# Kernel tuning notes

Hardware: AMD Instinct MI355X
Metric: run time of the kernel (lower is better)

## Reference

```python
import jax, jax.numpy as jnp
import numpy as np

V, E, H, T, B, L = 50000, 512, 1024, 21, 64, 256


def setup_inputs() -> dict:
    key = jax.random.key(0)
    ks = jax.random.split(key, 16)
    s = 0.05
    return {
        "input_ids": jax.random.randint(ks[0], (B, L), 0, V, dtype=jnp.int32),
        "tags": jax.random.randint(ks[1], (B, L), 0, T, dtype=jnp.int32),
        "mask": jnp.ones((B, L), dtype=bool),
        "embed_table": jax.random.normal(ks[2], (V, E), dtype=jnp.float32) * s,
        "W_ih_f": jax.random.normal(ks[3], (4 * H, E), dtype=jnp.float32) * s,
        "W_hh_f": jax.random.normal(ks[4], (4 * H, H), dtype=jnp.float32) * s,
        "b_ih_f": jnp.zeros((4 * H,), jnp.float32),
        "b_hh_f": jnp.zeros((4 * H,), jnp.float32),
        "W_ih_b": jax.random.normal(ks[5], (4 * H, E), dtype=jnp.float32) * s,
        "W_hh_b": jax.random.normal(ks[6], (4 * H, H), dtype=jnp.float32) * s,
        "b_ih_b": jnp.zeros((4 * H,), jnp.float32),
        "b_hh_b": jnp.zeros((4 * H,), jnp.float32),
        "W_out": jax.random.normal(ks[7], (T, 2 * H), dtype=jnp.float32) * s,
        "b_out": jnp.zeros((T,), jnp.float32),
        "start_trans": jax.random.uniform(ks[8], (T,), minval=-0.1, maxval=0.1),
        "end_trans": jax.random.uniform(ks[9], (T,), minval=-0.1, maxval=0.1),
        "transitions": jax.random.uniform(ks[10], (T, T), minval=-0.1, maxval=0.1),
    }


def _lstm_dir(x_proj, W_hh):
    # x_proj: [L, B, 4H] = x @ W_ih.T + b_ih + b_hh. PyTorch gate order i,f,g,o.
    Hh = W_hh.shape[1]
    Bn = x_proj.shape[1]

    def step(carry, xt):
        h, c = carry
        g = xt + h @ W_hh.T
        i, f, gg, o = jnp.split(g, 4, axis=-1)
        c = jax.nn.sigmoid(f) * c + jax.nn.sigmoid(i) * jnp.tanh(gg)
        h = jax.nn.sigmoid(o) * jnp.tanh(c)
        return (h, c), h

    init = (jnp.zeros((Bn, Hh), x_proj.dtype), jnp.zeros((Bn, Hh), x_proj.dtype))
    _, hs = jax.lax.scan(step, init, x_proj)
    return hs  # [L, B, H]


def reference(input_ids, tags, mask, embed_table, W_ih_f, W_hh_f, b_ih_f, b_hh_f,
              W_ih_b, W_hh_b, b_ih_b, b_hh_b, W_out, b_out,
              start_trans, end_trans, transitions):
    # Embedding (padding_idx=0 row is zero in torch)
    emb = embed_table.at[0].set(0.0)[input_ids]          # [B, L, E]
    x = jnp.swapaxes(emb, 0, 1)                          # [L, B, E]

    # BiLSTM: precompute input projections, scan each direction
    hs_f = _lstm_dir(x @ W_ih_f.T + b_ih_f + b_hh_f, W_hh_f)           # [L, B, H]
    hs_b = _lstm_dir(x[::-1] @ W_ih_b.T + b_ih_b + b_hh_b, W_hh_b)[::-1]
    emissions = jnp.concatenate([hs_f, hs_b], axis=-1) @ W_out.T + b_out  # [L, B, T]

    m = jnp.swapaxes(mask, 0, 1).astype(emissions.dtype)  # [L, B]
    tg = jnp.swapaxes(tags, 0, 1)                         # [L, B]

    # CRF numerator: gold path score
    em_t = jnp.take_along_axis(emissions, tg[:, :, None], axis=2)[..., 0]  # [L, B]
    tr_t = transitions[tg[:-1], tg[1:]]                                    # [L-1, B]
    num = start_trans[tg[0]] + em_t[0] + jnp.sum((tr_t + em_t[1:]) * m[1:], axis=0)
    last_idx = jnp.sum(m, axis=0).astype(jnp.int32) - 1                    # [B]
    last_tags = jnp.take_along_axis(tg, last_idx[None, :], axis=0)[0]
    num = num + end_trans[last_tags]

    # CRF partition function: forward algorithm over time
    def step(score, inp):
        em, mm = inp
        nxt = jax.nn.logsumexp(score[:, :, None] + transitions[None] + em[:, None, :], axis=1)
        return jnp.where(mm[:, None] > 0, nxt, score), None

    score0 = start_trans[None, :] + emissions[0]          # [B, T]
    score, _ = jax.lax.scan(step, score0, (emissions[1:], m[1:]))
    logZ = jax.nn.logsumexp(score + end_trans[None, :], axis=1)  # [B]

    # loss = -crf(emissions, tags, mask, reduction='mean')
    return -jnp.mean(num - logZ)
```

## Files before the change

kernel.cpp:

```cpp
#include <hip/hip_runtime.h>
#include <math.h>

#define VV 50000
#define EE 512
#define HH 1024
#define G4 4096
#define NT 21
#define NB 64
#define LL 256
#define KTOT 1536

typedef __attribute__((ext_vector_type(8))) short short8v;
typedef __attribute__((ext_vector_type(4))) float float4v;

__device__ __forceinline__ float sigf(float x){ return 1.f/(1.f+__expf(-x)); }

__device__ __forceinline__ float bf2f(unsigned short u){
  union { unsigned int i; float f; } v; v.i = ((unsigned int)u)<<16; return v.f;
}
__device__ __forceinline__ unsigned short f2bf(float f){
  union { float f; unsigned int u; } v; v.f = f;
  unsigned int u = v.u;
  u += 0x7FFFu + ((u >> 16) & 1u);
  return (unsigned short)(u >> 16);
}


__global__ void k_cast_weights(const float* __restrict__ Wih_f, const float* __restrict__ Whh_f,
                               const float* __restrict__ Wih_b, const float* __restrict__ Whh_b,
                               unsigned short* __restrict__ Wcat)
{
  int idx = blockIdx.x*256 + threadIdx.x;
  if (idx >= 2*4096*192) return;
  int dir = idx / (4096*192);
  int rem = idx - dir*(4096*192);
  int g   = rem / 192;
  int kc  = rem - g*192;
  const float* src;
  if (kc < 64) src = (dir ? Wih_b : Wih_f) + (size_t)g*EE + kc*8;
  else         src = (dir ? Whh_b : Whh_f) + (size_t)g*HH + (kc-64)*8;
  unsigned short tmp[8];
  #pragma unroll
  for (int e=0;e<8;e++) tmp[e] = f2bf(src[e]);
  *(uint4*)(Wcat + (size_t)(dir*G4 + g)*KTOT + kc*8) = *(const uint4*)tmp;
}

__global__ void k_bias(const float* bif, const float* bhf,
                       const float* bib, const float* bhb, float* bsum)
{
  int idx = blockIdx.x*256 + threadIdx.x;
  if (idx >= 2*G4) return;
  int d = idx >> 12, g = idx & (G4-1);
  bsum[idx] = d ? (bib[g]+bhb[g]) : (bif[g]+bhf[g]);
}

__global__ void k_embed(const int* __restrict__ ids, const float* __restrict__ table,
                        unsigned short* __restrict__ x)
{
  int tok = blockIdx.x;
  int t = tok >> 6, b = tok & 63;
  int id = ids[b*LL + t];
  int e0 = threadIdx.x*8;
  unsigned short tmp[8];
  if (id == 0) {
    #pragma unroll
    for (int e=0;e<8;e++) tmp[e] = 0;
  } else {
    const float* row = table + (size_t)id*EE + e0;
    #pragma unroll
    for (int e=0;e<8;e++) tmp[e] = f2bf(row[e]);
  }
  *(uint4*)(x + (size_t)tok*EE + e0) = *(const uint4*)tmp;
}

__global__ void k_zero(unsigned short* hsf0, unsigned short* hsb0, float* cst)
{
  int idx = blockIdx.x*256 + threadIdx.x;
  if (idx < NB*HH) { hsf0[idx] = 0; hsb0[idx] = 0; }
  if (idx < 2*NB*HH) cst[idx] = 0.f;
}

__global__ __launch_bounds__(256) void k_step(
    const unsigned short* __restrict__ Wcat, const float* __restrict__ bsum,
    const unsigned short* __restrict__ x,
    unsigned short* __restrict__ hs_f, unsigned short* __restrict__ hs_b,
    float* __restrict__ cst, int t)
{
  const int dir = blockIdx.x >> 6;
  const int j   = blockIdx.x & 63;
  const int tid = threadIdx.x;
  const int w = tid >> 6, lane = tid & 63;
  const int l15 = lane & 15, lg = lane >> 4;

  const int xtime = dir ? (LL-1 - t) : t;
  unsigned short* hbuf = dir ? hs_b : hs_f;
  const unsigned short* hprev = hbuf + (size_t)t*(NB*HH);
  unsigned short*       hnext = hbuf + (size_t)(t+1)*(NB*HH);
  const unsigned short* xt = x + (size_t)xtime*(NB*EE);

  const int gc0 = w*HH + j*16;
  const short8v* wp = (const short8v*)(Wcat + ((size_t)(dir*G4 + gc0 + l15))*KTOT + lg*8);

  float4v acc[4];
  #pragma unroll
  for (int mt=0;mt<4;mt++)
    #pragma unroll
    for (int i=0;i<4;i++) acc[mt][i] = 0.f;

  #pragma unroll 4
  for (int kt=0; kt<16; kt++) {
    short8v bfrag = wp[kt*4];
    #pragma unroll
    for (int mt=0; mt<4; mt++) {
      short8v afrag = *(const short8v*)(xt + (size_t)(mt*16 + l15)*EE + kt*32 + lg*8);
      acc[mt] = __builtin_amdgcn_mfma_f32_16x16x32_bf16(afrag, bfrag, acc[mt], 0, 0, 0);
    }
  }
  #pragma unroll 4
  for (int kt=0; kt<32; kt++) {
    short8v bfrag = wp[(16+kt)*4];
    #pragma unroll
    for (int mt=0; mt<4; mt++) {
      short8v afrag = *(const short8v*)(hprev + (size_t)(mt*16 + l15)*HH + kt*32 + lg*8);
      acc[mt] = __builtin_amdgcn_mfma_f32_16x16x32_bf16(afrag, bfrag, acc[mt], 0, 0, 0);
    }
  }

  __shared__ float gbuf[4][64][17];
  #pragma unroll
  for (int mt=0;mt<4;mt++)
    #pragma unroll
    for (int i=0;i<4;i++)
      gbuf[w][mt*16 + lg*4 + i][l15] = acc[mt][i];
  __syncthreads();

  const int colbase = j*16;
  #pragma unroll
  for (int k=0;k<4;k++){
    int e  = k*256 + tid;
    int b  = e >> 4, hc = e & 15;
    int col = colbase + hc;
    float gi = gbuf[0][b][hc] + bsum[dir*G4 + col];
    float gf = gbuf[1][b][hc] + bsum[dir*G4 + HH   + col];
    float gg = gbuf[2][b][hc] + bsum[dir*G4 + 2*HH + col];
    float go = gbuf[3][b][hc] + bsum[dir*G4 + 3*HH + col];
    size_t ci = (size_t)dir*(NB*HH) + (size_t)b*HH + col;
    float c0 = cst[ci];
    float cn = sigf(gf)*c0 + sigf(gi)*tanhf(gg);
    float hn = sigf(go)*tanhf(cn);
    cst[ci] = cn;
    hnext[(size_t)b*HH + col] = f2bf(hn);
  }
}

__global__ __launch_bounds__(256) void k_emis(
    const unsigned short* __restrict__ hs_f, const unsigned short* __restrict__ hs_b,
    const float* __restrict__ Wout, const float* __restrict__ bout,
    float* __restrict__ em)
{
  int wid = blockIdx.x*4 + (threadIdx.x >> 6);
  int lane = threadIdx.x & 63;
  int t = wid >> 6, b = wid & 63;

  const unsigned short* hf = hs_f + (size_t)(t+1)*(NB*HH) + (size_t)b*HH + lane*16;
  const unsigned short* hb = hs_b + (size_t)(LL-t)*(NB*HH) + (size_t)b*HH + lane*16;
  unsigned short uf[16], ub[16];
  *(uint4*)uf     = *(const uint4*)hf;
  *(uint4*)(uf+8) = *(const uint4*)(hf+8);
  *(uint4*)ub     = *(const uint4*)hb;
  *(uint4*)(ub+8) = *(const uint4*)(hb+8);
  float vf[16], vb[16];
  #pragma unroll
  for (int e=0;e<16;e++){ vf[e]=bf2f(uf[e]); vb[e]=bf2f(ub[e]); }

  for (int jj=0; jj<NT; jj++){
    const float* wr = Wout + (size_t)jj*(2*HH) + lane*16;
    float s = 0.f;
    #pragma unroll
    for (int e=0;e<16;e++) s += vf[e]*wr[e];
    const float* wr2 = wr + HH;
    #pragma unroll
    for (int e=0;e<16;e++) s += vb[e]*wr2[e];
    #pragma unroll
    for (int off=32; off; off>>=1) s += __shfl_down(s, off);
    if (lane==0) em[((size_t)t*NB + b)*NT + jj] = s + bout[jj];
  }
}

__global__ void k_num(const int* __restrict__ tags, const float* __restrict__ em,
                      const float* __restrict__ startt, const float* __restrict__ endt,
                      const float* __restrict__ trans, float* __restrict__ num)
{
  int b = threadIdx.x;
  const int* tg = tags + b*LL;
  int prev = tg[0];
  float acc = startt[prev] + em[(size_t)b*NT + prev];
  for (int t=1; t<LL; t++){
    int cur = tg[t];
    acc += trans[prev*NT + cur] + em[((size_t)t*NB + b)*NT + cur];
    prev = cur;
  }
  acc += endt[prev];
  num[b] = acc;
}

__global__ void k_logz(const float* __restrict__ em, const float* __restrict__ startt,
                       const float* __restrict__ endt, const float* __restrict__ trans,
                       float* __restrict__ logz)
{
  __shared__ float tl[NT*NT + 64];
  int b = blockIdx.x, j = threadIdx.x;
  for (int i=j; i<NT*NT; i+=64) tl[i] = trans[i];
  for (int i=NT*NT+j; i<NT*NT+64; i+=64) tl[i] = 0.f;
  __syncthreads();

  float score = (j < NT) ? (startt[j] + em[(size_t)b*NT + j]) : -1e30f;
  for (int t=1; t<LL; t++){
    float m = -1e30f, s = 0.f;
    #pragma unroll 7
    for (int i=0; i<NT; i++){
      float v = __shfl(score, i) + tl[i*NT + j];
      float mn = fmaxf(m, v);
      s = s*__expf(m-mn) + __expf(v-mn);
      m = mn;
    }
    float ns = em[((size_t)t*NB + b)*NT + j] + m + __logf(s);
    score = (j < NT) ? ns : -1e30f;
  }
  float v = (j < NT) ? (score + endt[j]) : -1e30f;
  float mx = v;
  #pragma unroll
  for (int off=32; off; off>>=1) mx = fmaxf(mx, __shfl_xor(mx, off));
  float s = __expf(v - mx);
  #pragma unroll
  for (int off=32; off; off>>=1) s += __shfl_xor(s, off);
  if (j==0) logz[b] = mx + __logf(s);
}

__global__ void k_final(const float* num, const float* logz, float* out)
{
  int b = threadIdx.x;
  float v = num[b] - logz[b];
  #pragma unroll
  for (int off=32; off; off>>=1) v += __shfl_xor(v, off);
  if (b==0) out[0] = -(v / (float)NB);
}

extern "C" void kernel_launch(void* const* d_in, const int* in_sizes, int n_in,
                              void* d_out, int out_size, void* d_ws, size_t ws_size,
                              hipStream_t stream)
{
  const int*   ids    = (const int*)  d_in[0];
  const int*   tags   = (const int*)  d_in[1];
  const float* table  = (const float*)d_in[3];
  const float* Wih_f  = (const float*)d_in[4];
  const float* Whh_f  = (const float*)d_in[5];
  const float* bif    = (const float*)d_in[6];
  const float* bhf    = (const float*)d_in[7];
  const float* Wih_b  = (const float*)d_in[8];
  const float* Whh_b  = (const float*)d_in[9];
  const float* bib    = (const float*)d_in[10];
  const float* bhb    = (const float*)d_in[11];
  const float* Wout   = (const float*)d_in[12];
  const float* bout   = (const float*)d_in[13];
  const float* startt = (const float*)d_in[14];
  const float* endt   = (const float*)d_in[15];
  const float* trans  = (const float*)d_in[16];
  float* out = (float*)d_out;

  char* p = (char*)d_ws;
  auto alloc = [&](size_t bytes)->char* {
    char* r = p; p += (bytes + 255) & ~(size_t)255; return r;
  };
  unsigned short* Wcat = (unsigned short*)alloc((size_t)2*G4*KTOT*2);
  float*          bsum = (float*)         alloc((size_t)2*G4*4);
  unsigned short* x    = (unsigned short*)alloc((size_t)LL*NB*EE*2);
  unsigned short* hs_f = (unsigned short*)alloc((size_t)(LL+1)*NB*HH*2);
  unsigned short* hs_b = (unsigned short*)alloc((size_t)(LL+1)*NB*HH*2);
  float*          cst  = (float*)         alloc((size_t)2*NB*HH*4);
  float*          em   = (float*)         alloc((size_t)LL*NB*NT*4);
  float*          num  = (float*)         alloc(64*4);
  float*          logz = (float*)         alloc(64*4);
  (void)ws_size; (void)in_sizes; (void)n_in; (void)out_size;

  k_cast_weights<<<(2*4096*192 + 255)/256, 256, 0, stream>>>(Wih_f, Whh_f, Wih_b, Whh_b, Wcat);
  k_bias<<<(2*G4 + 255)/256, 256, 0, stream>>>(bif, bhf, bib, bhb, bsum);
  k_embed<<<LL*NB, 64, 0, stream>>>(ids, table, x);
  k_zero<<<(2*NB*HH + 255)/256, 256, 0, stream>>>(hs_f, hs_b, cst);

  for (int t = 0; t < LL; t++)
    k_step<<<128, 256, 0, stream>>>(Wcat, bsum, x, hs_f, hs_b, cst, t);

  k_emis<<<(LL*NB)/4, 256, 0, stream>>>(hs_f, hs_b, Wout, bout, em);
  k_num<<<1, 64, 0, stream>>>(tags, em, startt, endt, trans, num);
  k_logz<<<64, 64, 0, stream>>>(em, startt, endt, trans, logz);
  k_final<<<1, 64, 0, stream>>>(num, logz, out);
}
```

Baseline: 8.666 ms.

## Replace per-timestep LSTM launches with persistent kernel using grid barriers and LDS weights

The 256 per-timestep kernel launches become a single persistent kernel of 256 blocks, one group of 128 blocks per direction. Each block keeps its 32-column slice of the gate weights resident in LDS, holds the cell state in registers, and synchronises each step with a spin-based grid barrier. The emission projection is also rewritten to use bf16 MFMA with Wout staged in LDS. This removes launch overhead and repeated weight reads from global memory. In exchange it depends on all 256 blocks being co-resident, and the barrier gives up after a spin timeout, which could silently break ordering.

```diff
diff --git a/kernel.cpp b/kernel.cpp
--- a/kernel.cpp
+++ b/kernel.cpp
@@ -9,6 +9,11 @@
 #define NB 64
 #define LL 256
 #define KTOT 1536
+
+#define WSTRIDE 1544
+#define SMEM_P (32*WSTRIDE*2 + 64*36*4)
+#define ESTRIDE 2056
+#define SMEM_E (32*ESTRIDE*2)
 
 typedef __attribute__((ext_vector_type(8))) short short8v;
 typedef __attribute__((ext_vector_type(4))) float float4v;
@@ -73,117 +78,190 @@
   *(uint4*)(x + (size_t)tok*EE + e0) = *(const uint4*)tmp;
 }
 
-__global__ void k_zero(unsigned short* hsf0, unsigned short* hsb0, float* cst)
+__global__ void k_zero(unsigned short* hsf0, unsigned short* hsb0, int* bar)
 {
   int idx = blockIdx.x*256 + threadIdx.x;
   if (idx < NB*HH) { hsf0[idx] = 0; hsb0[idx] = 0; }
-  if (idx < 2*NB*HH) cst[idx] = 0.f;
-}
-
-__global__ __launch_bounds__(256) void k_step(
+  if (idx < 64) bar[idx] = 0;
+}
+
+__device__ __forceinline__ void grid_barrier(int* cnt, int* gen, int nb)
+{
+  __syncthreads();
+  if (threadIdx.x == 0){
+    __threadfence();
+    int g = __hip_atomic_load(gen, __ATOMIC_RELAXED, __HIP_MEMORY_SCOPE_AGENT);
+    int arrived = __hip_atomic_fetch_add(cnt, 1, __ATOMIC_ACQ_REL, __HIP_MEMORY_SCOPE_AGENT);
+    if (arrived == nb - 1){
+      __hip_atomic_store(cnt, 0, __ATOMIC_RELAXED, __HIP_MEMORY_SCOPE_AGENT);
+      __hip_atomic_fetch_add(gen, 1, __ATOMIC_RELEASE, __HIP_MEMORY_SCOPE_AGENT);
+    } else {
+      long spins = 0;
+      while (__hip_atomic_load(gen, __ATOMIC_ACQUIRE, __HIP_MEMORY_SCOPE_AGENT) == g){
+        __builtin_amdgcn_s_sleep(2);
+        if (++spins > 2000000L) break;
+      }
+    }
+  }
+  __syncthreads();
+}
+
+__global__ __launch_bounds__(256, 1) void k_persist(
     const unsigned short* __restrict__ Wcat, const float* __restrict__ bsum,
     const unsigned short* __restrict__ x,
-    unsigned short* __restrict__ hs_f, unsigned short* __restrict__ hs_b,
-    float* __restrict__ cst, int t)
-{
-  const int dir = blockIdx.x >> 6;
-  const int j   = blockIdx.x & 63;
+    unsigned short* hs_f, unsigned short* hs_b, int* bar)
+{
+  extern __shared__ char smem[];
+  unsigned short* Wl  = (unsigned short*)smem;
+  float*          gbuf = (float*)(smem + 32*WSTRIDE*2);
+
+  const int dir = blockIdx.x >> 7;
+  const int j   = blockIdx.x & 127;
   const int tid = threadIdx.x;
   const int w = tid >> 6, lane = tid & 63;
   const int l15 = lane & 15, lg = lane >> 4;
-
-  const int xtime = dir ? (LL-1 - t) : t;
+  const int tile = w >> 1, mtb = (w & 1) * 2;
+
   unsigned short* hbuf = dir ? hs_b : hs_f;
-  const unsigned short* hprev = hbuf + (size_t)t*(NB*HH);
-  unsigned short*       hnext = hbuf + (size_t)(t+1)*(NB*HH);
-  const unsigned short* xt = x + (size_t)xtime*(NB*EE);
-
-  const int gc0 = w*HH + j*16;
-  const short8v* wp = (const short8v*)(Wcat + ((size_t)(dir*G4 + gc0 + l15))*KTOT + lg*8);
-
-  float4v acc[4];
-  #pragma unroll
-  for (int mt=0;mt<4;mt++)
+  int* cnt = bar + dir*32;
+  int* gen = cnt + 16;
+
+  for (int n = 0; n < 32; n++){
+    int gcol = ((n >> 3) << 10) + j*8 + (n & 7);
+    const unsigned short* src = Wcat + ((size_t)(dir*G4 + gcol))*KTOT;
+    if (tid < 192)
+      *(uint4*)&Wl[n*WSTRIDE + tid*8] = *(const uint4*)&src[tid*8];
+  }
+
+  const int e0 = tid*2;
+  const int b0 = e0 >> 3, hc0 = e0 & 7;
+  const int colg = j*8;
+  float bi[2], bff[2], bg[2], bo[2];
+  #pragma unroll
+  for (int r=0;r<2;r++){
+    int c = colg + hc0 + r;
+    bi[r]  = bsum[dir*G4 + c];
+    bff[r] = bsum[dir*G4 + HH   + c];
+    bg[r]  = bsum[dir*G4 + 2*HH + c];
+    bo[r]  = bsum[dir*G4 + 3*HH + c];
+  }
+  float creg[2] = {0.f, 0.f};
+
+  const unsigned short* wt = Wl + (tile*16 + l15)*WSTRIDE + lg*8;
+  const int arow0 = mtb*16 + l15;
+  __syncthreads();
+
+  for (int t = 0; t < LL; t++){
+    const int xtime = dir ? (LL-1-t) : t;
+    const unsigned short* xr0 = x    + (size_t)xtime*(NB*EE) + (size_t)arow0*EE + lg*8;
+    const unsigned short* hr0 = hbuf + (size_t)t*(NB*HH)     + (size_t)arow0*HH + lg*8;
+
+    float4v acc0 = {0,0,0,0}, acc1 = {0,0,0,0};
+    #pragma unroll 4
+    for (int kt=0; kt<16; kt++){
+      short8v bfrag = *(const short8v*)(wt + kt*32);
+      short8v a0 = *(const short8v*)(xr0 + kt*32);
+      short8v a1 = *(const short8v*)(xr0 + 16*EE + kt*32);
+      acc0 = __builtin_amdgcn_mfma_f32_16x16x32_bf16(a0, bfrag, acc0, 0,0,0);
+      acc1 = __builtin_amdgcn_mfma_f32_16x16x32_bf16(a1, bfrag, acc1, 0,0,0);
+    }
+    #pragma unroll 4
+    for (int kt=0; kt<32; kt++){
+      short8v bfrag = *(const short8v*)(wt + (16+kt)*32);
+      short8v a0 = *(const short8v*)(hr0 + kt*32);
+      short8v a1 = *(const short8v*)(hr0 + 16*HH + kt*32);
+      acc0 = __builtin_amdgcn_mfma_f32_16x16x32_bf16(a0, bfrag, acc0, 0,0,0);
+      acc1 = __builtin_amdgcn_mfma_f32_16x16x32_bf16(a1, bfrag, acc1, 0,0,0);
+    }
+
     #pragma unroll
-    for (int i=0;i<4;i++) acc[mt][i] = 0.f;
-
-  #pragma unroll 4
-  for (int kt=0; kt<16; kt++) {
-    short8v bfrag = wp[kt*4];
+    for (int i=0;i<4;i++){
+      gbuf[(mtb*16     + lg*4 + i)*36 + tile*16 + l15] = acc0[i];
+      gbuf[((mtb+1)*16 + lg*4 + i)*36 + tile*16 + l15] = acc1[i];
+    }
+    __syncthreads();
+
+    unsigned short* hnext = hbuf + (size_t)(t+1)*(NB*HH);
+    unsigned short hh2[2];
     #pragma unroll
-    for (int mt=0; mt<4; mt++) {
-      short8v afrag = *(const short8v*)(xt + (size_t)(mt*16 + l15)*EE + kt*32 + lg*8);
-      acc[mt] = __builtin_amdgcn_mfma_f32_16x16x32_bf16(afrag, bfrag, acc[mt], 0, 0, 0);
-    }
-  }
-  #pragma unroll 4
-  for (int kt=0; kt<32; kt++) {
-    short8v bfrag = wp[(16+kt)*4];
-    #pragma unroll
-    for (int mt=0; mt<4; mt++) {
-      short8v afrag = *(const short8v*)(hprev + (size_t)(mt*16 + l15)*HH + kt*32 + lg*8);
-      acc[mt] = __builtin_amdgcn_mfma_f32_16x16x32_bf16(afrag, bfrag, acc[mt], 0, 0, 0);
-    }
-  }
-
-  __shared__ float gbuf[4][64][17];
-  #pragma unroll
-  for (int mt=0;mt<4;mt++)
-    #pragma unroll
-    for (int i=0;i<4;i++)
-      gbuf[w][mt*16 + lg*4 + i][l15] = acc[mt][i];
-  __syncthreads();
-
-  const int colbase = j*16;
-  #pragma unroll
-  for (int k=0;k<4;k++){
-    int e  = k*256 + tid;
-    int b  = e >> 4, hc = e & 15;
-    int col = colbase + hc;
-    float gi = gbuf[0][b][hc] + bsum[dir*G4 + col];
-    float gf = gbuf[1][b][hc] + bsum[dir*G4 + HH   + col];
-    float gg = gbuf[2][b][hc] + bsum[dir*G4 + 2*HH + col];
-    float go = gbuf[3][b][hc] + bsum[dir*G4 + 3*HH + col];
-    size_t ci = (size_t)dir*(NB*HH) + (size_t)b*HH + col;
-    float c0 = cst[ci];
-    float cn = sigf(gf)*c0 + sigf(gi)*tanhf(gg);
-    float hn = sigf(go)*tanhf(cn);
-    cst[ci] = cn;
-    hnext[(size_t)b*HH + col] = f2bf(hn);
-  }
-}
-
-__global__ __launch_bounds__(256) void k_emis(
+    for (int r=0;r<2;r++){
+      int hc = hc0 + r;
+      float gi = gbuf[b0*36 + hc]      + bi[r];
+      float gf = gbuf[b0*36 + 8 + hc]  + bff[r];
+      float gg = gbuf[b0*36 + 16 + hc] + bg[r];
+      float go = gbuf[b0*36 + 24 + hc] + bo[r];
+      float c = sigf(gf)*creg[r] + sigf(gi)*tanhf(gg);
+      float h = sigf(go)*tanhf(c);
+      creg[r] = c;
+      hh2[r] = f2bf(h);
+    }
+    *(unsigned int*)&hnext[(size_t)b0*HH + colg + hc0] =
+        ((unsigned int)hh2[1] << 16) | (unsigned int)hh2[0];
+
+    grid_barrier(cnt, gen, 128);
+  }
+}
+
+__global__ __launch_bounds__(256, 1) void k_emis2(
     const unsigned short* __restrict__ hs_f, const unsigned short* __restrict__ hs_b,
     const float* __restrict__ Wout, const float* __restrict__ bout,
     float* __restrict__ em)
 {
-  int wid = blockIdx.x*4 + (threadIdx.x >> 6);
-  int lane = threadIdx.x & 63;
-  int t = wid >> 6, b = wid & 63;
-
-  const unsigned short* hf = hs_f + (size_t)(t+1)*(NB*HH) + (size_t)b*HH + lane*16;
-  const unsigned short* hb = hs_b + (size_t)(LL-t)*(NB*HH) + (size_t)b*HH + lane*16;
-  unsigned short uf[16], ub[16];
-  *(uint4*)uf     = *(const uint4*)hf;
-  *(uint4*)(uf+8) = *(const uint4*)(hf+8);
-  *(uint4*)ub     = *(const uint4*)hb;
-  *(uint4*)(ub+8) = *(const uint4*)(hb+8);
-  float vf[16], vb[16];
-  #pragma unroll
-  for (int e=0;e<16;e++){ vf[e]=bf2f(uf[e]); vb[e]=bf2f(ub[e]); }
-
-  for (int jj=0; jj<NT; jj++){
-    const float* wr = Wout + (size_t)jj*(2*HH) + lane*16;
-    float s = 0.f;
-    #pragma unroll
-    for (int e=0;e<16;e++) s += vf[e]*wr[e];
-    const float* wr2 = wr + HH;
-    #pragma unroll
-    for (int e=0;e<16;e++) s += vb[e]*wr2[e];
-    #pragma unroll
-    for (int off=32; off; off>>=1) s += __shfl_down(s, off);
-    if (lane==0) em[((size_t)t*NB + b)*NT + jj] = s + bout[jj];
+  extern __shared__ char smem[];
+  unsigned short* Wl = (unsigned short*)smem;
+
+  const int t = blockIdx.x;
+  const int tid = threadIdx.x;
+  const int w = tid>>6, lane = tid&63, l15 = lane&15, lg = lane>>4;
+
+  for (int c=0;c<32;c++){
+    unsigned short v8[8];
+    if (c < NT){
+      const float* src = Wout + (size_t)c*(2*HH) + tid*8;
+      #pragma unroll
+      for (int e=0;e<8;e++) v8[e] = f2bf(src[e]);
+    } else {
+      #pragma unroll
+      for (int e=0;e<8;e++) v8[e] = 0;
+    }
+    *(uint4*)&Wl[c*ESTRIDE + tid*8] = *(const uint4*)v8;
+  }
+  __syncthreads();
+
+  const int b = w*16 + l15;
+  const unsigned short* hf = hs_f + (size_t)(t+1)*(NB*HH)  + (size_t)b*HH + lg*8;
+  const unsigned short* hb = hs_b + (size_t)(LL-t)*(NB*HH) + (size_t)b*HH + lg*8;
+
+  float4v acc0 = {0,0,0,0}, acc1 = {0,0,0,0};
+  #pragma unroll 4
+  for (int kt=0;kt<32;kt++){
+    short8v a  = *(const short8v*)(hf + kt*32);
+    short8v bf0 = *(const short8v*)(Wl + (size_t)l15*ESTRIDE      + kt*32 + lg*8);
+    short8v bf1 = *(const short8v*)(Wl + (size_t)(16+l15)*ESTRIDE + kt*32 + lg*8);
+    acc0 = __builtin_amdgcn_mfma_f32_16x16x32_bf16(a, bf0, acc0, 0,0,0);
+    acc1 = __builtin_amdgcn_mfma_f32_16x16x32_bf16(a, bf1, acc1, 0,0,0);
+  }
+  #pragma unroll 4
+  for (int kt=0;kt<32;kt++){
+    short8v a  = *(const short8v*)(hb + kt*32);
+    short8v bf0 = *(const short8v*)(Wl + (size_t)l15*ESTRIDE      + (32+kt)*32 + lg*8);
+    short8v bf1 = *(const short8v*)(Wl + (size_t)(16+l15)*ESTRIDE + (32+kt)*32 + lg*8);
+    acc0 = __builtin_amdgcn_mfma_f32_16x16x32_bf16(a, bf0, acc0, 0,0,0);
+    acc1 = __builtin_amdgcn_mfma_f32_16x16x32_bf16(a, bf1, acc1, 0,0,0);
+  }
+
+  #pragma unroll
+  for (int nt=0;nt<2;nt++){
+    int tag = nt*16 + l15;
+    if (tag < NT){
+      float bb = bout[tag];
+      const float4v accv = nt ? acc1 : acc0;
+      #pragma unroll
+      for (int i=0;i<4;i++){
+        int bo_ = w*16 + lg*4 + i;
+        em[((size_t)t*NB + bo_)*NT + tag] = accv[i] + bb;
+      }
+    }
   }
 }
 
@@ -277,21 +355,25 @@
   unsigned short* x    = (unsigned short*)alloc((size_t)LL*NB*EE*2);
   unsigned short* hs_f = (unsigned short*)alloc((size_t)(LL+1)*NB*HH*2);
   unsigned short* hs_b = (unsigned short*)alloc((size_t)(LL+1)*NB*HH*2);
-  float*          cst  = (float*)         alloc((size_t)2*NB*HH*4);
   float*          em   = (float*)         alloc((size_t)LL*NB*NT*4);
   float*          num  = (float*)         alloc(64*4);
   float*          logz = (float*)         alloc(64*4);
+  int*            bar  = (int*)           alloc(64*4);
   (void)ws_size; (void)in_sizes; (void)n_in; (void)out_size;
 
   k_cast_weights<<<(2*4096*192 + 255)/256, 256, 0, stream>>>(Wih_f, Whh_f, Wih_b, Whh_b, Wcat);
   k_bias<<<(2*G4 + 255)/256, 256, 0, stream>>>(bif, bhf, bib, bhb, bsum);
   k_embed<<<LL*NB, 64, 0, stream>>>(ids, table, x);
-  k_zero<<<(2*NB*HH + 255)/256, 256, 0, stream>>>(hs_f, hs_b, cst);
-
-  for (int t = 0; t < LL; t++)
-    k_step<<<128, 256, 0, stream>>>(Wcat, bsum, x, hs_f, hs_b, cst, t);
-
-  k_emis<<<(LL*NB)/4, 256, 0, stream>>>(hs_f, hs_b, Wout, bout, em);
+  k_zero<<<(NB*HH + 255)/256, 256, 0, stream>>>(hs_f, hs_b, bar);
+
+  (void)hipFuncSetAttribute((const void*)k_persist,
+        hipFuncAttributeMaxDynamicSharedMemorySize, SMEM_P);
+  k_persist<<<256, 256, SMEM_P, stream>>>(Wcat, bsum, x, hs_f, hs_b, bar);
+
+  (void)hipFuncSetAttribute((const void*)k_emis2,
+        hipFuncAttributeMaxDynamicSharedMemorySize, SMEM_E);
+  k_emis2<<<LL, 256, SMEM_E, stream>>>(hs_f, hs_b, Wout, bout, em);
+
   k_num<<<1, 64, 0, stream>>>(tags, em, startt, endt, trans, num);
   k_logz<<<64, 64, 0, stream>>>(em, startt, endt, trans, logz);
   k_final<<<1, 64, 0, stream>>>(num, logz, out);
```

New measurement: 9.842 ms. 1.14x slower.
